# Performance work log

Hardware: AMD Instinct MI355X
Metric: run time of the kernel (lower is better)

Reference implementation:

```python
import jax, jax.numpy as jnp
import numpy as np

CODEBOOK_SIZE = 128
EMBED_DIM = 32
LATENT_SIZE = 8
BATCH = 32768


def setup_inputs() -> dict:
    key = jax.random.key(0)
    k1, k2 = jax.random.split(key)
    latent = jax.random.normal(k1, (BATCH, LATENT_SIZE, EMBED_DIM), dtype=jnp.float32)
    # original init: uniform(-1/codebook_size, 1/codebook_size)
    codebook = jax.random.uniform(k2, (CODEBOOK_SIZE, EMBED_DIM), dtype=jnp.float32,
                                  minval=-1.0 / CODEBOOK_SIZE, maxval=1.0 / CODEBOOK_SIZE)
    return {"latent": latent, "codebook": codebook}


def reference(latent, codebook):
    B = latent.shape[0]
    K, D = codebook.shape
    flat = latent.reshape(-1, D)  # [N, D]
    # squared euclidean distances [N, K]
    distances = (jnp.sum(flat ** 2, axis=-1, keepdims=True)
                 + jnp.sum(codebook ** 2, axis=-1)
                 - 2.0 * flat @ codebook.T)
    encoding_indices = jnp.argmin(distances, axis=-1)  # [N]
    # one-hot @ codebook == direct gather
    quantized_latent = codebook[encoding_indices].reshape(latent.shape)
    # straight-through estimator
    policy_vq_latent = latent + jax.lax.stop_gradient(quantized_latent - latent)
    codebook_set = jnp.broadcast_to(codebook[None], (B, K, D))
    return (policy_vq_latent, quantized_latent, codebook_set)
```

## Files before the change

### kernel.cpp

```cpp
#include <hip/hip_runtime.h>


typedef float f32x4 __attribute__((ext_vector_type(4)));

constexpr int N_ROWS    = 32768 * 8;
constexpr int KCODES    = 128;
constexpr int DIM       = 32;
constexpr int THREADS   = 256;
constexpr int VQ_BLOCKS = N_ROWS / THREADS;
constexpr int BC_BLOCKS = 2048;
constexpr long long QUANT_OFF = (long long)N_ROWS * DIM;
constexpr long long CBSET_OFF = 2LL * N_ROWS * DIM;
constexpr int CBSET_F4 = (int)(32768LL * 128 * 32 / 4);
constexpr int PERIOD_F4_MASK = 1023;

__global__ __launch_bounds__(THREADS)
void vq_fused_kernel(const float* __restrict__ latent,
                     const float* __restrict__ codebook,
                     float* __restrict__ out) {
#pragma clang fp contract(off)
    __shared__ float s_cb[KCODES * DIM];
    __shared__ float s_c2[KCODES];

    const int tid = threadIdx.x;
    const int bid = blockIdx.x;

    if (bid < VQ_BLOCKS) {
        {
            f32x4* s4 = (f32x4*)s_cb;
            const f32x4* g4 = (const f32x4*)codebook;
            #pragma unroll
            for (int j = 0; j < (KCODES * DIM / 4) / THREADS; ++j)
                s4[tid + THREADS * j] = g4[tid + THREADS * j];
        }
        __syncthreads();

        if (tid < KCODES) {
            const float* c = &s_cb[tid * DIM];
            float t[DIM];
            #pragma unroll
            for (int d = 0; d < DIM; ++d) t[d] = c[d] * c[d];
            float r[8];
            #pragma unroll
            for (int j = 0; j < 8; ++j)
                r[j] = ((t[j] + t[j + 8]) + t[j + 16]) + t[j + 24];
            s_c2[tid] = ((r[0] + r[1]) + (r[2] + r[3])) + ((r[4] + r[5]) + (r[6] + r[7]));
        }
        __syncthreads();

        const int row = bid * THREADS + tid;
        const f32x4* x4 = (const f32x4*)latent + (size_t)row * 8;

        float x2[DIM];
        float S;
        {
            float t[DIM];
            #pragma unroll
            for (int j = 0; j < 8; ++j) {
                f32x4 v = x4[j];
                #pragma unroll
                for (int e = 0; e < 4; ++e) {
                    float xv = v[e];
                    t[4 * j + e]  = xv * xv;
                    x2[4 * j + e] = 2.0f * xv;
                }
            }
            float r[8];
            #pragma unroll
            for (int j = 0; j < 8; ++j)
                r[j] = ((t[j] + t[j + 8]) + t[j + 16]) + t[j + 24];
            S = ((r[0] + r[1]) + (r[2] + r[3])) + ((r[4] + r[5]) + (r[6] + r[7]));
        }

        float best = 3.402823466e38f;
        int bestk = 0;
        const f32x4* c4 = (const f32x4*)s_cb;
        #pragma unroll 4
        for (int k = 0; k < KCODES; ++k) {
            float acc = 0.0f;
            #pragma unroll
            for (int j = 0; j < 8; ++j) {
                f32x4 cv = c4[k * 8 + j];
                #pragma unroll
                for (int e = 0; e < 4; ++e) {
                    float prod = x2[4 * j + e] * cv[e];
                    acc = acc + prod;
                }
            }
            float dist = (S + s_c2[k]) - acc;
            if (dist < best) { best = dist; bestk = k; }
        }

        f32x4* pol = (f32x4*)out + (size_t)row * 8;
        f32x4* qnt = (f32x4*)(out + QUANT_OFF) + (size_t)row * 8;
        const f32x4* q4 = (const f32x4*)&s_cb[bestk * DIM];
        #pragma unroll
        for (int j = 0; j < 8; ++j) {
            f32x4 q = q4[j];
            f32x4 p;
            #pragma unroll
            for (int e = 0; e < 4; ++e) {
                float xv = 0.5f * x2[4 * j + e];
                p[e] = xv + (q[e] - xv);
            }
            pol[j] = p;
            qnt[j] = q;
        }
    } else {
        const int btid = (bid - VQ_BLOCKS) * THREADS + tid;
        const int stride = BC_BLOCKS * THREADS;
        const f32x4* g4 = (const f32x4*)codebook;
        f32x4* o4 = (f32x4*)(out + CBSET_OFF);
        for (int i = btid; i < CBSET_F4; i += stride) {
            f32x4 v = g4[i & PERIOD_F4_MASK];
            __builtin_nontemporal_store(v, &o4[i]);
        }
    }
}

extern "C" void kernel_launch(void* const* d_in, const int* in_sizes, int n_in,
                              void* d_out, int out_size, void* d_ws, size_t ws_size,
                              hipStream_t stream) {
    const float* latent   = (const float*)d_in[0];
    const float* codebook = (const float*)d_in[1];
    float* out = (float*)d_out;
    vq_fused_kernel<<<dim3(VQ_BLOCKS + BC_BLOCKS), dim3(THREADS), 0, stream>>>(
        latent, codebook, out);
}
```

Baseline: 609.3 us.

## Process four rows per thread to reuse codebook LDS loads across rows

Each thread now handles four latent rows. Every codebook vector read from shared memory is reused for four distance computations, which cuts LDS traffic per row. The VQ block count drops by four, the broadcast block count is raised to rebalance the grid, and the VQ outputs now use nontemporal stores. The cost is much higher register pressure (four 32-float rows held in registers), which may lower occupancy, and each thread's row accesses become more strided, which hurts coalescing.

```diff
diff --git a/kernel.cpp b/kernel.cpp
--- a/kernel.cpp
+++ b/kernel.cpp
@@ -7,8 +7,9 @@
 constexpr int KCODES    = 128;
 constexpr int DIM       = 32;
 constexpr int THREADS   = 256;
-constexpr int VQ_BLOCKS = N_ROWS / THREADS;
-constexpr int BC_BLOCKS = 2048;
+constexpr int RPT       = 4;
+constexpr int VQ_BLOCKS = N_ROWS / (THREADS * RPT);
+constexpr int BC_BLOCKS = 2816;
 constexpr long long QUANT_OFF = (long long)N_ROWS * DIM;
 constexpr long long CBSET_OFF = 2LL * N_ROWS * DIM;
 constexpr int CBSET_F4 = (int)(32768LL * 128 * 32 / 4);
@@ -48,12 +49,13 @@
         }
         __syncthreads();
 
-        const int row = bid * THREADS + tid;
-        const f32x4* x4 = (const f32x4*)latent + (size_t)row * 8;
+        const int row0 = (bid * THREADS + tid) * RPT;
 
-        float x2[DIM];
-        float S;
-        {
+        float x2[RPT][DIM];
+        float S[RPT];
+        #pragma unroll
+        for (int rr = 0; rr < RPT; ++rr) {
+            const f32x4* x4 = (const f32x4*)latent + (size_t)(row0 + rr) * 8;
             float t[DIM];
             #pragma unroll
             for (int j = 0; j < 8; ++j) {
@@ -61,50 +63,62 @@
                 #pragma unroll
                 for (int e = 0; e < 4; ++e) {
                     float xv = v[e];
-                    t[4 * j + e]  = xv * xv;
-                    x2[4 * j + e] = 2.0f * xv;
+                    t[4 * j + e]        = xv * xv;
+                    x2[rr][4 * j + e]   = 2.0f * xv;
                 }
             }
             float r[8];
             #pragma unroll
             for (int j = 0; j < 8; ++j)
                 r[j] = ((t[j] + t[j + 8]) + t[j + 16]) + t[j + 24];
-            S = ((r[0] + r[1]) + (r[2] + r[3])) + ((r[4] + r[5]) + (r[6] + r[7]));
+            S[rr] = ((r[0] + r[1]) + (r[2] + r[3])) + ((r[4] + r[5]) + (r[6] + r[7]));
         }
 
-        float best = 3.402823466e38f;
-        int bestk = 0;
+        float best[RPT];
+        int   bestk[RPT];
+        #pragma unroll
+        for (int rr = 0; rr < RPT; ++rr) { best[rr] = 3.402823466e38f; bestk[rr] = 0; }
+
         const f32x4* c4 = (const f32x4*)s_cb;
-        #pragma unroll 4
+        #pragma unroll 2
         for (int k = 0; k < KCODES; ++k) {
-            float acc = 0.0f;
+            f32x4 cv[8];
+            #pragma unroll
+            for (int j = 0; j < 8; ++j) cv[j] = c4[k * 8 + j];
+            const float c2k = s_c2[k];
+            #pragma unroll
+            for (int rr = 0; rr < RPT; ++rr) {
+                float acc = 0.0f;
+                #pragma unroll
+                for (int j = 0; j < 8; ++j) {
+                    #pragma unroll
+                    for (int e = 0; e < 4; ++e) {
+                        float prod = x2[rr][4 * j + e] * cv[e == 0 ? j : j][e];
+                        acc = acc + prod;
+                    }
+                }
+                float dist = (S[rr] + c2k) - acc;
+                if (dist < best[rr]) { best[rr] = dist; bestk[rr] = k; }
+            }
+        }
+
+        #pragma unroll
+        for (int rr = 0; rr < RPT; ++rr) {
+            f32x4* pol = (f32x4*)out + (size_t)(row0 + rr) * 8;
+            f32x4* qnt = (f32x4*)(out + QUANT_OFF) + (size_t)(row0 + rr) * 8;
+            const f32x4* q4 = (const f32x4*)&s_cb[bestk[rr] * DIM];
             #pragma unroll
             for (int j = 0; j < 8; ++j) {
-                f32x4 cv = c4[k * 8 + j];
+                f32x4 q = q4[j];
+                f32x4 p;
                 #pragma unroll
                 for (int e = 0; e < 4; ++e) {
-                    float prod = x2[4 * j + e] * cv[e];
-                    acc = acc + prod;
+                    float xv = 0.5f * x2[rr][4 * j + e];
+                    p[e] = xv + (q[e] - xv);
                 }
+                __builtin_nontemporal_store(p, &pol[j]);
+                __builtin_nontemporal_store(q, &qnt[j]);
             }
-            float dist = (S + s_c2[k]) - acc;
-            if (dist < best) { best = dist; bestk = k; }
-        }
-
-        f32x4* pol = (f32x4*)out + (size_t)row * 8;
-        f32x4* qnt = (f32x4*)(out + QUANT_OFF) + (size_t)row * 8;
-        const f32x4* q4 = (const f32x4*)&s_cb[bestk * DIM];
-        #pragma unroll
-        for (int j = 0; j < 8; ++j) {
-            f32x4 q = q4[j];
-            f32x4 p;
-            #pragma unroll
-            for (int e = 0; e < 4; ++e) {
-                float xv = 0.5f * x2[4 * j + e];
-                p[e] = xv + (q[e] - xv);
-            }
-            pol[j] = p;
-            qnt[j] = q;
         }
     } else {
         const int btid = (bid - VQ_BLOCKS) * THREADS + tid;
```

After: 813.1 us. 1.33x slower.
